# Optimization experiments

Hardware: AMD Instinct MI355X
Metric: run time of the kernel (lower is better)

The kernel has to match this reference:

```python
import jax, jax.numpy as jnp
import numpy as np

DEPTH, DIM, DIN, DM, NST, RNK, CSTEM, NCLS = 4, 64, 128, 256, 16, 8, 32, 16
EPS = 1e-5


def silu(x):
    return x * jax.nn.sigmoid(x)


def layernorm(x, g, b):
    m = x.mean(-1, keepdims=True)
    v = x.var(-1, keepdims=True)
    return (x - m) / jnp.sqrt(v + EPS) * g + b


def bn3d(x, g, b, m, v):  # eval-mode BatchNorm3d, x [B,C,T,H,W]
    s = g / jnp.sqrt(v + EPS)
    return x * s[None, :, None, None, None] + (b - m * s)[None, :, None, None, None]


def dwconv3d_same(x, w, b):  # x [B,C,T,H,W], w [C,1,3,3,3]
    y = jax.lax.conv_general_dilated(x, w, (1, 1, 1), 'SAME',
                                     feature_group_count=x.shape[1],
                                     dimension_numbers=('NCDHW', 'OIDHW', 'NCDHW'))
    return y + b[None, :, None, None, None]


def mamba(u, in_w, conv_w, conv_b, xproj_w, dtproj_w, dtproj_b, Alog, Dp, out_w):
    # u: [b, L, DIN]; mamba_ssm Mamba(d_model=DIN, d_state=16, expand=2, d_conv=4)
    b, L, _ = u.shape
    xz = u @ in_w.T                                  # [b,L,2*DM]
    x, z = jnp.split(xz, 2, axis=-1)                 # [b,L,DM] each
    # causal depthwise conv1d, kernel 4, left-pad 3
    xc = jnp.moveaxis(x, 1, 2)                       # [b,DM,L]
    xc = jnp.pad(xc, ((0, 0), (0, 0), (3, 0)))
    xc = jax.lax.conv_general_dilated(xc, conv_w, (1,), 'VALID',
                                      feature_group_count=conv_w.shape[0],
                                      dimension_numbers=('NCH', 'OIH', 'NCH'))
    xc = xc + conv_b[None, :, None]
    x = silu(jnp.moveaxis(xc, 2, 1))                 # [b,L,DM]
    dbc = x @ xproj_w.T                              # [b,L,RNK+2*NST]
    dt, Bc, Cc = jnp.split(dbc, [RNK, RNK + NST], axis=-1)
    dt = jax.nn.softplus(dt @ dtproj_w.T + dtproj_b)  # [b,L,DM]
    A = -jnp.exp(Alog)                               # [DM,NST]

    def step(h, inp):
        dt_l, u_l, B_l, C_l = inp                    # [b,DM],[b,DM],[b,NST],[b,NST]
        dA = jnp.exp(dt_l[..., None] * A)            # [b,DM,NST]
        h = dA * h + (dt_l * u_l)[..., None] * B_l[:, None, :]
        y = jnp.einsum('bdn,bn->bd', h, C_l)
        return h, y

    xs = (jnp.moveaxis(dt, 1, 0), jnp.moveaxis(x, 1, 0),
          jnp.moveaxis(Bc, 1, 0), jnp.moveaxis(Cc, 1, 0))
    h0 = jnp.zeros((b, DM, NST), x.dtype)
    _, ys = jax.lax.scan(step, h0, xs)               # ys [L,b,DM]
    y = jnp.moveaxis(ys, 0, 1) + x * Dp              # D skip
    y = y * silu(z)
    return y @ out_w.T                               # [b,L,DIN]


def setup_inputs() -> dict:
    key = jax.random.key(0)
    ks = iter(jax.random.split(key, 64))

    def rn(shape, s=0.02):
        return jax.random.normal(next(ks), shape, jnp.float32) * s

    D = DEPTH
    inp = {
        'x': jax.random.normal(next(ks), (32, 1, 32, 13, 13), jnp.float32),
        # R(2+1)D stem
        'sconv_w': rn((CSTEM, 1, 1, 3, 3), 0.1),
        'bn1_g': jnp.ones((CSTEM,)), 'bn1_b': jnp.zeros((CSTEM,)),
        'bn1_m': rn((CSTEM,), 0.1),
        'bn1_v': jax.random.uniform(next(ks), (CSTEM,), jnp.float32, 0.5, 1.5),
        'tconv_w': rn((CSTEM, 1, 3, 1, 1), 0.2),
        'bn2_g': jnp.ones((CSTEM,)), 'bn2_b': jnp.zeros((CSTEM,)),
        'bn2_m': rn((CSTEM,), 0.1),
        'bn2_v': jax.random.uniform(next(ks), (CSTEM,), jnp.float32, 0.5, 1.5),
        'last_w': rn((2 * CSTEM, CSTEM, 1, 1, 1), 0.1),
        # per-block params, stacked over depth
        'ln1_g': jnp.ones((D, DIM)), 'ln1_b': jnp.zeros((D, DIM)),
        'in_proj_w': rn((D, 2 * DIN, DIM)),
        'conv3d_w': rn((D, DIN, 1, 3, 3, 3), 0.1), 'conv3d_b': rn((D, DIN), 0.1),
        'm_in_w': rn((D, 2 * DM, DIN)),
        'm_conv_w': rn((D, DM, 1, 4), 0.2), 'm_conv_b': rn((D, DM), 0.1),
        'm_xproj_w': rn((D, RNK + 2 * NST, DM)),
        'm_dtproj_w': rn((D, DM, RNK), 0.1), 'm_dtproj_b': rn((D, DM), 0.1),
        'm_Alog': jnp.log(jax.random.uniform(next(ks), (D, DM, NST), jnp.float32, 1.0, 16.0)),
        'm_D': jnp.ones((D, DM)),
        'm_out_w': rn((D, DIN, DM)),
        'out_proj_w': rn((D, DIM, DIN)),
        'ln2_g': jnp.ones((D, DIM)), 'ln2_b': jnp.zeros((D, DIM)),
        'fc1_w': rn((D, 4 * DIM, DIM)), 'fc1_b': rn((D, 4 * DIM), 0.1),
        'fc2_w': rn((D, DIM, 4 * DIM)), 'fc2_b': rn((D, DIM), 0.1),
        'head_w': rn((NCLS, DIM)), 'head_b': jnp.zeros((NCLS,)),
    }
    return inp


def reference(x, sconv_w, bn1_g, bn1_b, bn1_m, bn1_v, tconv_w, bn2_g, bn2_b, bn2_m,
              bn2_v, last_w, ln1_g, ln1_b, in_proj_w, conv3d_w, conv3d_b, m_in_w,
              m_conv_w, m_conv_b, m_xproj_w, m_dtproj_w, m_dtproj_b, m_Alog, m_D,
              m_out_w, out_proj_w, ln2_g, ln2_b, fc1_w, fc1_b, fc2_w, fc2_b,
              head_w, head_b):
    dn = ('NCDHW', 'OIDHW', 'NCDHW')
    # R(2+1)D stem: spatial conv -> BN -> ReLU -> temporal dwconv -> BN -> ReLU -> 1x1x1
    h = jax.lax.conv_general_dilated(x, sconv_w, (1, 1, 1), 'VALID', dimension_numbers=dn)
    h = jax.nn.relu(bn3d(h, bn1_g, bn1_b, bn1_m, bn1_v))
    h = jax.lax.conv_general_dilated(h, tconv_w, (1, 1, 1), 'VALID',
                                     feature_group_count=CSTEM, dimension_numbers=dn)
    h = jax.nn.relu(bn3d(h, bn2_g, bn2_b, bn2_m, bn2_v))
    h = jax.lax.conv_general_dilated(h, last_w, (1, 1, 1), 'VALID', dimension_numbers=dn)
    xb = jnp.transpose(h, (0, 2, 3, 4, 1))  # [B, T', H', W', DIM]

    for i in range(DEPTH):
        # --- SSM branch ---
        hx = layernorm(xb, ln1_g[i], ln1_b[i])
        xz = hx @ in_proj_w[i].T                       # [B,T,H,W,2*DIN]
        xs_, z = jnp.split(xz, 2, axis=-1)
        z = silu(z)
        xc = jnp.moveaxis(xs_, 4, 1)                   # [B,DIN,T,H,W]
        xc = silu(dwconv3d_same(xc, conv3d_w[i], conv3d_b[i]))
        b, c, t, hh, ww = xc.shape
        seq = jnp.moveaxis(xc.reshape(b, c, t * hh * ww), 1, 2)  # [B,L,DIN]
        seq2 = jnp.concatenate([seq, seq[:, ::-1]], axis=0)      # [2B,L,DIN]
        y2 = mamba(seq2, m_in_w[i], m_conv_w[i], m_conv_b[i], m_xproj_w[i],
                   m_dtproj_w[i], m_dtproj_b[i], m_Alog[i], m_D[i], m_out_w[i])
        y = y2[:b] + y2[b:, ::-1]
        y = y.reshape(b, t, hh, ww, c) * z
        xb = xb + y @ out_proj_w[i].T
        # --- MLP branch ---
        h2 = layernorm(xb, ln2_g[i], ln2_b[i])
        h2 = jax.nn.gelu(h2 @ fc1_w[i].T + fc1_b[i], approximate=False)
        xb = xb + h2 @ fc2_w[i].T + fc2_b[i]

    feature = xb.mean(axis=(1, 2, 3))                  # [B, DIM]
    logits = feature @ head_w.T + head_b               # [B, NCLS]
    return (logits, feature)
```

## Files before the change

kernel.cpp:

```cpp
#include <hip/hip_runtime.h>
#include <hip/hip_bf16.h>
#include <hip/hip_fp16.h>

#define LL    3630
#define EPSV  1e-5f
#define NCH   57
#define CLEN  64

typedef short bf16x8 __attribute__((ext_vector_type(8)));
typedef float f32x4  __attribute__((ext_vector_type(4)));
typedef float f32x2  __attribute__((ext_vector_type(2)));
typedef float f32x16 __attribute__((ext_vector_type(16)));

__device__ __forceinline__ float bf2f(__hip_bfloat16 x){ return __bfloat162float(x); }
__device__ __forceinline__ __hip_bfloat16 f2bf(float x){ return __float2bfloat16(x); }
__device__ __forceinline__ float siluf(float x){ return x / (1.f + __expf(-x)); }
__device__ __forceinline__ float s2f(short s){ __hip_bfloat16 t = __builtin_bit_cast(__hip_bfloat16, s); return __bfloat162float(t); }
__device__ __forceinline__ short f2s(float x){ __hip_bfloat16 t = __float2bfloat16(x); return __builtin_bit_cast(short, t); }

__global__ __launch_bounds__(256) void convert_weights(
    const float* __restrict__ s0, const float* __restrict__ s1,
    const float* __restrict__ s2, const float* __restrict__ s3,
    const float* __restrict__ s4, const float* __restrict__ s5,
    const float* __restrict__ s6,
    __hip_bfloat16* __restrict__ dst)
{
  int gid = blockIdx.x*256 + threadIdx.x;
  float v;
  if      (gid <  65536) v = s0[gid];
  else if (gid < 327680) v = s1[gid-65536];
  else if (gid < 458752) v = s2[gid-327680];
  else if (gid < 491520) v = s3[gid-458752];
  else if (gid < 557056) v = s4[gid-491520];
  else if (gid < 622592) v = s5[gid-557056];
  else if (gid < 671744){
    int rel = gid - 622592;
    int layer = rel / 12288;
    int rr  = (rel % 12288) / 256;
    int ccol= rel & 255;
    v = (rr < 40) ? s6[layer*10240 + rr*256 + ccol] : 0.f;
  }
  else return;
  dst[gid] = f2bf(v);
}

__global__ __launch_bounds__(256) void stem1_kernel(
    const float* __restrict__ x, const float* __restrict__ w,
    const float* __restrict__ g, const float* __restrict__ bb,
    const float* __restrict__ mm, const float* __restrict__ vv,
    float* __restrict__ out, int nb, int b0)
{
  int idx = blockIdx.x*256 + threadIdx.x;
  if (idx >= nb*123904) return;
  int j = idx % 11;
  int i = (idx/11) % 11;
  int t = (idx/121) % 32;
  int c = (idx/(121*32)) % 32;
  int b = idx/(121*32*32);
  const float* xp = x + ((b0+b)*32 + t)*169;
  const float* wp = w + c*9;
  float acc = 0.f;
  #pragma unroll
  for (int di=0; di<3; ++di)
    #pragma unroll
    for (int dj=0; dj<3; ++dj)
      acc += xp[(i+di)*13 + (j+dj)] * wp[di*3+dj];
  float s = g[c]*rsqrtf(vv[c]+EPSV);
  acc = acc*s + (bb[c]-mm[c]*s);
  out[idx] = fmaxf(acc, 0.f);
}

__global__ __launch_bounds__(256) void stem2_kernel(
    const float* __restrict__ h1, const float* __restrict__ w,
    const float* __restrict__ g, const float* __restrict__ bb,
    const float* __restrict__ mm, const float* __restrict__ vv,
    float* __restrict__ out, int nb)
{
  int idx = blockIdx.x*256 + threadIdx.x;
  if (idx >= nb*116160) return;
  int ij = idx % 121;
  int t  = (idx/121) % 30;
  int c  = (idx/(121*30)) % 32;
  int b  = idx/(121*30*32);
  const float* hp = h1 + ((b*32+c)*32)*121 + ij;
  const float* wp = w + c*3;
  float acc = 0.f;
  #pragma unroll
  for (int k=0;k<3;++k) acc += hp[(t+k)*121] * wp[k];
  float s = g[c]*rsqrtf(vv[c]+EPSV);
  acc = acc*s + (bb[c]-mm[c]*s);
  out[idx] = fmaxf(acc, 0.f);
}

__global__ __launch_bounds__(256) void stem3_kernel(
    const float* __restrict__ h2, const float* __restrict__ w,
    __hip_bfloat16* __restrict__ xb, int tokens)
{
  int gid = blockIdx.x*256 + threadIdx.x;
  int cc = gid & 63;
  int tok = gid >> 6;
  if (tok >= tokens) return;
  int ij = tok % 121;
  int t  = (tok/121) % 30;
  int b  = tok/LL;
  const float* hp = h2 + ((long)b*32)*30*121 + t*121 + ij;
  const float* wp = w + cc*32;
  float acc = 0.f;
  #pragma unroll
  for (int ci=0; ci<32; ++ci) acc += hp[ci*3630] * wp[ci];
  xb[(long)tok*64+cc] = f2bf(acc);
}

__global__ __launch_bounds__(256) void ln_kernel(
    const __hip_bfloat16* __restrict__ xb, const float* __restrict__ g,
    const float* __restrict__ b2, __hip_bfloat16* __restrict__ out, int tokens)
{
  int wid = threadIdx.x >> 6, lane = threadIdx.x & 63;
  long tok = (long)blockIdx.x*4 + wid;
  if (tok >= tokens) return;
  float v = bf2f(xb[tok*64 + lane]);
  float s = v, q = v*v;
  #pragma unroll
  for (int m=1; m<64; m<<=1){ s += __shfl_xor(s,m); q += __shfl_xor(q,m); }
  float mean = s*(1.f/64.f);
  float var  = q*(1.f/64.f) - mean*mean;
  float o = (v-mean)*rsqrtf(var+EPSV)*g[lane] + b2[lane];
  out[tok*64+lane] = f2bf(o);
}

template<int EPI>
__global__ __launch_bounds__(256) void gemm_bf16(
    const __hip_bfloat16* __restrict__ A, const __hip_bfloat16* __restrict__ W,
    int K, int N, int NH, int ny, int tokens,
    __hip_bfloat16* __restrict__ out1, __hip_bfloat16* __restrict__ out2,
    const float* __restrict__ bias, const __hip_bfloat16* __restrict__ gate,
    __hip_bfloat16* __restrict__ resid,
    const float* __restrict__ lng, const float* __restrict__ lnb)
{
  int w   = threadIdx.x >> 6;
  int lane= threadIdx.x & 63;
  int r16 = lane & 15;
  int kg  = lane >> 4;
  int nwg = gridDim.x;
  int orig = blockIdx.x;
  int q = nwg >> 3, r8 = nwg & 7;
  int xcd = orig & 7, off = orig >> 3;
  int wg = (xcd < r8 ? xcd*(q+1) : r8*(q+1) + (xcd-r8)*q) + off;
  int by = wg % ny;
  long bx = wg / ny;
  long m0 = bx*128 + w*32;
  int  n0 = by*64;
  long ra0 = m0 + r16;      if (ra0 > tokens-1) ra0 = tokens-1;
  long ra1 = m0 + 16 + r16; if (ra1 > tokens-1) ra1 = tokens-1;
  f32x4 acc[2][4] = { { {0,0,0,0},{0,0,0,0},{0,0,0,0},{0,0,0,0} },
                      { {0,0,0,0},{0,0,0,0},{0,0,0,0},{0,0,0,0} } };
  for (int k0 = 0; k0 < K; k0 += 32){
    bf16x8 a0 = *reinterpret_cast<const bf16x8*>(A + ra0*K + k0 + kg*8);
    bf16x8 a1 = *reinterpret_cast<const bf16x8*>(A + ra1*K + k0 + kg*8);
    #pragma unroll
    for (int f=0; f<4; ++f){
      bf16x8 b = *reinterpret_cast<const bf16x8*>(W + (long)(n0 + f*16 + r16)*K + k0 + kg*8);
      acc[0][f] = __builtin_amdgcn_mfma_f32_16x16x32_bf16(a0, b, acc[0][f], 0, 0, 0);
      acc[1][f] = __builtin_amdgcn_mfma_f32_16x16x32_bf16(a1, b, acc[1][f], 0, 0, 0);
    }
  }
  if (EPI == 5){
    float gv[4], bv[4], biasv[4];
    #pragma unroll
    for (int f=0; f<4; ++f){
      gv[f] = lng[f*16+r16]; bv[f] = lnb[f*16+r16];
      biasv[f] = bias ? bias[f*16+r16] : 0.f;
    }
    #pragma unroll
    for (int g2=0; g2<2; ++g2){
      #pragma unroll
      for (int r=0; r<4; ++r){
        long row = m0 + g2*16 + kg*4 + r;
        bool ok = row < tokens;
        long rowc = ok ? row : (tokens-1);
        float v[4]; float s = 0.f, qq = 0.f;
        #pragma unroll
        for (int f=0; f<4; ++f){
          float t = acc[g2][f][r] + biasv[f] + bf2f(resid[rowc*64 + f*16+r16]);
          v[f] = t; s += t; qq += t*t;
        }
        #pragma unroll
        for (int m=1; m<16; m<<=1){ s += __shfl_xor(s,m); qq += __shfl_xor(qq,m); }
        float mean = s*(1.f/64.f);
        float var  = qq*(1.f/64.f) - mean*mean;
        float rstd = rsqrtf(var+EPSV);
        if (ok){
          #pragma unroll
          for (int f=0; f<4; ++f){
            resid[row*64 + f*16+r16] = f2bf(v[f]);
            out1 [row*64 + f*16+r16] = f2bf((v[f]-mean)*rstd*gv[f] + bv[f]);
          }
        }
      }
    }
    return;
  }
  #pragma unroll
  for (int g2=0; g2<2; ++g2){
    #pragma unroll
    for (int f=0; f<4; ++f){
      int col = n0 + f*16 + r16;
      #pragma unroll
      for (int r=0; r<4; ++r){
        long row = m0 + g2*16 + kg*4 + r;
        if (row >= tokens) continue;
        float v = acc[g2][f][r];
        if (EPI == 0){
          if (col < NH) out1[row*NH + col] = f2bf(v);
          else          out2[row*NH + col - NH] = f2bf(siluf(v));
        } else if (EPI == 2){
          v += bias[col];
          v = 0.5f*v*(1.f + erff(v*0.70710678118f));
          out1[row*N + col] = f2bf(v);
        } else {
          out1[row*N + col] = f2bf(v * bf2f(gate[row*N + col]));
        }
      }
    }
  }
}

__global__ __launch_bounds__(256) void dwconv3d_kernel(
    const __hip_bfloat16* __restrict__ xs, const float* __restrict__ w,
    const float* __restrict__ bias, __hip_bfloat16* __restrict__ seq, int tokens)
{
  long gid = (long)blockIdx.x*256 + threadIdx.x;
  int c = gid & 127;
  long tok = gid >> 7;
  if (tok >= tokens) return;
  int j  = tok % 11;
  int i2 = (tok/11) % 11;
  int t  = (tok/121) % 30;
  long b = tok/LL;
  const float* wc = w + c*27;
  float acc = bias[c];
  #pragma unroll
  for (int dt=0; dt<3; ++dt){
    int tt = t+dt-1; if (tt<0 || tt>=30) continue;
    #pragma unroll
    for (int di=0; di<3; ++di){
      int ii = i2+di-1; if (ii<0 || ii>=11) continue;
      #pragma unroll
      for (int dj=0; dj<3; ++dj){
        int jj = j+dj-1; if (jj<0 || jj>=11) continue;
        long t2 = (b*30+tt)*121 + ii*11 + jj;
        acc += wc[dt*9+di*3+dj] * bf2f(xs[t2*128 + c]);
      }
    }
  }
  seq[tok*128 + c] = f2bf(siluf(acc));
}

__global__ __launch_bounds__(256) void mamba_pre_scan(
    const __hip_bfloat16* __restrict__ xm,
    const float* __restrict__ cw, const float* __restrict__ cbv,
    const __hip_bfloat16* __restrict__ xpw_bf,
    const float* __restrict__ dtw, const float* __restrict__ dtbv,
    const float* __restrict__ Alog,
    __hip_bfloat16* __restrict__ ub,
    float* __restrict__ pre,
    float* __restrict__ hfin, float* __restrict__ sdt,
    int nb)
{
  __shared__ __hip_bfloat16 xcs[64][264];
  __shared__ float pres[64][44];
  int s  = blockIdx.x / NCH;
  int ch = blockIdx.x % NCH;
  int p0 = ch*CLEN;
  int b  = s % nb;
  bool fwd = s < nb;
  int d = threadIdx.x;
  const long basex = (long)b*LL*256 + d;
  const long sLL = (long)s*LL;
  {
    float w0=cw[d*4], w1=cw[d*4+1], w2=cw[d*4+2], w3=cw[d*4+3], cb=cbv[d];
    float p1=0.f, p2=0.f, p3=0.f;
    if (p0-1 >= 0) p1 = bf2f(xm[basex + (long)(fwd ? p0-1 : LL-p0  )*256]);
    if (p0-2 >= 0) p2 = bf2f(xm[basex + (long)(fwd ? p0-2 : LL+1-p0)*256]);
    if (p0-3 >= 0) p3 = bf2f(xm[basex + (long)(fwd ? p0-3 : LL+2-p0)*256]);
    for (int t=0; t<64; ++t){
      int p = p0 + t;
      float xl = 0.f;
      if (p < LL) xl = bf2f(xm[basex + (long)(fwd ? p : LL-1-p)*256]);
      float xc = w3*xl + w2*p1 + w1*p2 + w0*p3 + cb;
      p3=p2; p2=p1; p1=xl;
      __hip_bfloat16 uv = f2bf(siluf(xc));
      xcs[t][d] = uv;
      if (p < LL) ub[(sLL + p)*256 + d] = uv;
    }
  }
  __syncthreads();
  {
    int w = threadIdx.x >> 6, lane = threadIdx.x & 63;
    int r16 = lane & 15, kg = lane >> 4;
    int t0 = w*16;
    f32x4 acc[3] = { {0,0,0,0},{0,0,0,0},{0,0,0,0} };
    for (int k0=0; k0<256; k0+=32){
      bf16x8 a = *reinterpret_cast<const bf16x8*>(&xcs[t0+r16][k0+kg*8]);
      #pragma unroll
      for (int f=0; f<3; ++f){
        bf16x8 bb = *reinterpret_cast<const bf16x8*>(xpw_bf + (f*16+r16)*256 + k0 + kg*8);
        acc[f] = __builtin_amdgcn_mfma_f32_16x16x32_bf16(a, bb, acc[f], 0, 0, 0);
      }
    }
    #pragma unroll
    for (int f=0; f<3; ++f){
      int col = f*16 + r16;
      #pragma unroll
      for (int r=0; r<4; ++r){
        int tl = t0 + kg*4 + r;
        int p = p0 + tl;
        if (col < 40){
          pres[tl][col] = acc[f][r];
          if (p < LL) pre[(sLL + p)*40 + col] = acc[f][r];
        }
      }
    }
  }
  __syncthreads();
  {
    int lim = LL - p0; if (lim > CLEN) lim = CLEN;
    f32x2 a2[8], h[8];
    #pragma unroll
    for (int k=0;k<8;++k){
      a2[k] = (f32x2){ -__expf(Alog[d*16+2*k])*1.44269504f,
                       -__expf(Alog[d*16+2*k+1])*1.44269504f };
      h[k] = (f32x2){0.f, 0.f};
    }
    float dw[8];
    #pragma unroll
    for (int r=0;r<8;++r) dw[r] = dtw[d*8+r];
    float dtb_d = dtbv[d];
    float sacc = 0.f;
    for (int t=0; t<lim; ++t){
      float u = bf2f(xcs[t][d]);
      float4 r0 = *reinterpret_cast<const float4*>(&pres[t][0]);
      float4 r1 = *reinterpret_cast<const float4*>(&pres[t][4]);
      float xacc = dtb_d;
      xacc = fmaf(r0.x,dw[0],fmaf(r0.y,dw[1],fmaf(r0.z,dw[2],fmaf(r0.w,dw[3],xacc))));
      xacc = fmaf(r1.x,dw[4],fmaf(r1.y,dw[5],fmaf(r1.z,dw[6],fmaf(r1.w,dw[7],xacc))));
      float dt = (xacc > 20.f) ? xacc : __logf(1.f + __expf(xacc));
      sacc += dt;
      float4 B0 = *reinterpret_cast<const float4*>(&pres[t][8]);
      float4 B1 = *reinterpret_cast<const float4*>(&pres[t][12]);
      float4 B2 = *reinterpret_cast<const float4*>(&pres[t][16]);
      float4 B3 = *reinterpret_cast<const float4*>(&pres[t][20]);
      float Bv[16] = {B0.x,B0.y,B0.z,B0.w,B1.x,B1.y,B1.z,B1.w,
                      B2.x,B2.y,B2.z,B2.w,B3.x,B3.y,B3.z,B3.w};
      f32x2 dt2  = (f32x2){dt, dt};
      float dtu = dt*u;
      f32x2 dtu2 = (f32x2){dtu, dtu};
      #pragma unroll
      for (int k=0;k<8;++k){
        f32x2 tt = dt2*a2[k];
        f32x2 e = (f32x2){ exp2f(tt.x), exp2f(tt.y) };
        f32x2 bk = (f32x2){ Bv[2*k], Bv[2*k+1] };
        h[k] = __builtin_elementwise_fma(e, h[k], dtu2*bk);
      }
    }
    long hbase = ((long)blockIdx.x*256 + d)*16;
    #pragma unroll
    for (int k=0;k<8;++k){ hfin[hbase+2*k] = h[k].x; hfin[hbase+2*k+1] = h[k].y; }
    sdt[(long)blockIdx.x*256 + d] = sacc;
  }
}

__global__ __launch_bounds__(256) void scan_comb(
    const float* __restrict__ Alog,
    float* __restrict__ hfin, const float* __restrict__ sdt)
{
  int s = blockIdx.x >> 4, dg = blockIdx.x & 15;
  int d = dg*16 + (threadIdx.x >> 4), n = threadIdx.x & 15;
  float a2 = -__expf(Alog[d*16+n]) * 1.44269504f;
  float h = 0.f;
  for (int ch=0; ch<NCH; ++ch){
    long sc = (long)s*NCH + ch;
    long idx = (sc*256 + d)*16 + n;
    float hf = hfin[idx];
    float sd = sdt[sc*256 + d];
    hfin[idx] = h;
    h = exp2f(a2*sd)*h + hf;
  }
}

__global__ __launch_bounds__(256) void scan_p2(
    __hip_bfloat16* __restrict__ ub,
    const float* __restrict__ pre,
    const float* __restrict__ dtw, const float* __restrict__ dtbv,
    const float* __restrict__ Alog, const float* __restrict__ Dv,
    const float* __restrict__ hinit)
{
  int d = threadIdx.x;
  int sc = blockIdx.x;
  int ch = sc % NCH, s = sc / NCH;
  int l0 = ch*CLEN;
  int lim = LL - l0; if (lim > CLEN) lim = CLEN;
  f32x2 a2[8], h[8];
  long hbase = ((long)sc*256 + d)*16;
  #pragma unroll
  for (int k=0;k<8;++k){
    a2[k] = (f32x2){ -__expf(Alog[d*16+2*k])*1.44269504f,
                     -__expf(Alog[d*16+2*k+1])*1.44269504f };
    h[k] = (f32x2){ hinit[hbase+2*k], hinit[hbase+2*k+1] };
  }
  float dw[8];
  #pragma unroll
  for (int r=0;r<8;++r) dw[r] = dtw[d*8+r];
  float dtb_d = dtbv[d];
  float dpv = Dv[d];
  long tok0 = (long)s*LL + l0;
  long ui = tok0*256 + d;
  long pi = tok0*40;
  for (int l=0; l<lim; ++l){
    float u = bf2f(ub[ui]);
    float4 r0 = *reinterpret_cast<const float4*>(pre+pi);
    float4 r1 = *reinterpret_cast<const float4*>(pre+pi+4);
    float xacc = dtb_d;
    xacc = fmaf(r0.x,dw[0],fmaf(r0.y,dw[1],fmaf(r0.z,dw[2],fmaf(r0.w,dw[3],xacc))));
    xacc = fmaf(r1.x,dw[4],fmaf(r1.y,dw[5],fmaf(r1.z,dw[6],fmaf(r1.w,dw[7],xacc))));
    float dt = (xacc > 20.f) ? xacc : __logf(1.f + __expf(xacc));
    f32x16 B = *reinterpret_cast<const f32x16*>(pre+pi+8);
    f32x16 C = *reinterpret_cast<const f32x16*>(pre+pi+24);
    f32x2 dt2  = (f32x2){dt, dt};
    float dtu = dt*u;
    f32x2 dtu2 = (f32x2){dtu, dtu};
    f32x2 y2 = (f32x2){0.f, 0.f};
    #pragma unroll
    for (int k=0;k<8;++k){
      f32x2 t = dt2*a2[k];
      f32x2 e = (f32x2){ exp2f(t.x), exp2f(t.y) };
      f32x2 bk = (f32x2){ B[2*k], B[2*k+1] };
      f32x2 ck = (f32x2){ C[2*k], C[2*k+1] };
      h[k] = __builtin_elementwise_fma(e, h[k], dtu2*bk);
      y2 = __builtin_elementwise_fma(h[k], ck, y2);
    }
    float y = y2.x + y2.y;
    ub[ui] = f2bf(y + u*dpv);
    ui += 256; pi += 40;
  }
}

__global__ __launch_bounds__(256) void combine_kernel(
    const __hip_bfloat16* __restrict__ yb, const __hip_bfloat16* __restrict__ zm,
    __hip_bfloat16* __restrict__ ycomb, int tokens, int nb)
{
  long gid = (long)blockIdx.x*256 + threadIdx.x;
  long tok = gid >> 5;
  if (tok >= tokens) return;
  int c8 = (gid & 31) * 8;
  long l = tok % LL, b = tok / LL;
  bf16x8 vf = *reinterpret_cast<const bf16x8*>(yb + ( b*LL + l)*256 + c8);
  bf16x8 vb = *reinterpret_cast<const bf16x8*>(yb + ((nb+b)*LL + (LL-1-l))*256 + c8);
  bf16x8 zz = *reinterpret_cast<const bf16x8*>(zm + tok*256 + c8);
  bf16x8 out;
  #pragma unroll
  for (int k=0;k<8;++k){
    float r = (s2f(vf[k]) + s2f(vb[k])) * s2f(zz[k]);
    out[k] = f2s(r);
  }
  *reinterpret_cast<bf16x8*>(ycomb + tok*256 + c8) = out;
}

__global__ __launch_bounds__(256) void head1_kernel(
    const __hip_bfloat16* __restrict__ xb, float* __restrict__ hp)
{
  __shared__ float partial[4][64];
  int b = blockIdx.x / 30, ch = blockIdx.x % 30;
  int d = threadIdx.x & 63, part = threadIdx.x >> 6;
  float acc = 0.f;
  int lend = (ch+1)*121;
  for (int l = ch*121 + part; l < lend; l += 4)
    acc += bf2f(xb[((long)b*LL + l)*64 + d]);
  partial[part][d] = acc;
  __syncthreads();
  if (part == 0)
    hp[(b*30 + ch)*64 + d] = partial[0][d]+partial[1][d]+partial[2][d]+partial[3][d];
}

__global__ __launch_bounds__(64) void head2_kernel(
    const float* __restrict__ hp, const float* __restrict__ hw,
    const float* __restrict__ hb, float* __restrict__ out, int b0)
{
  __shared__ float feat[64];
  int b = blockIdx.x;
  int d = threadIdx.x;
  float acc = 0.f;
  #pragma unroll
  for (int ch=0; ch<30; ++ch) acc += hp[(b*30+ch)*64 + d];
  float f = acc * (1.f/3630.f);
  feat[d] = f;
  out[512 + (b0+b)*64 + d] = f;
  __syncthreads();
  if (d < 16){
    float a2 = hb[d];
    #pragma unroll
    for (int k=0; k<64; ++k) a2 += feat[k]*hw[d*64+k];
    out[(b0+b)*16 + d] = a2;
  }
}

extern "C" void kernel_launch(void* const* d_in, const int* in_sizes, int n_in,
                              void* d_out, int out_size, void* d_ws, size_t ws_size,
                              hipStream_t stream)
{
  const float* x        = (const float*)d_in[0];
  const float* sconv_w  = (const float*)d_in[1];
  const float* bn1_g    = (const float*)d_in[2];
  const float* bn1_b    = (const float*)d_in[3];
  const float* bn1_m    = (const float*)d_in[4];
  const float* bn1_v    = (const float*)d_in[5];
  const float* tconv_w  = (const float*)d_in[6];
  const float* bn2_g    = (const float*)d_in[7];
  const float* bn2_b    = (const float*)d_in[8];
  const float* bn2_m    = (const float*)d_in[9];
  const float* bn2_v    = (const float*)d_in[10];
  const float* last_w   = (const float*)d_in[11];
  const float* ln1_g    = (const float*)d_in[12];
  const float* ln1_b    = (const float*)d_in[13];
  const float* in_proj_w= (const float*)d_in[14];
  const float* conv3d_w = (const float*)d_in[15];
  const float* conv3d_b = (const float*)d_in[16];
  const float* m_in_w   = (const float*)d_in[17];
  const float* m_conv_w = (const float*)d_in[18];
  const float* m_conv_b = (const float*)d_in[19];
  const float* m_xproj_w= (const float*)d_in[20];
  const float* m_dtproj_w=(const float*)d_in[21];
  const float* m_dtproj_b=(const float*)d_in[22];
  const float* m_Alog   = (const float*)d_in[23];
  const float* m_D      = (const float*)d_in[24];
  const float* m_out_w  = (const float*)d_in[25];
  const float* out_proj_w=(const float*)d_in[26];
  const float* ln2_g    = (const float*)d_in[27];
  const float* ln2_b    = (const float*)d_in[28];
  const float* fc1_w    = (const float*)d_in[29];
  const float* fc1_b    = (const float*)d_in[30];
  const float* fc2_w    = (const float*)d_in[31];
  const float* fc2_b    = (const float*)d_in[32];
  const float* head_w   = (const float*)d_in[33];
  const float* head_b   = (const float*)d_in[34];

  const size_t WB = 1345536;
  int nb = 1;
  for (int cand = 32; cand >= 1; cand >>= 1){
    size_t TPc = (((size_t)cand*LL + 63)/64)*64;
    size_t S2c = (size_t)2*cand*LL;
    size_t need = WB + TPc*2048 + S2c*672;
    if (need <= ws_size){ nb = cand; break; }
  }
  const size_t TP  = (((size_t)nb*LL + 63)/64)*64;
  const int S2  = 2*nb;
  const size_t S2T = (size_t)S2*LL;
  const int tokens = nb*LL;

  char* ws = (char*)d_ws;
  __hip_bfloat16* wbf   = (__hip_bfloat16*)(ws);
  size_t o = WB;
  __hip_bfloat16* xb    = (__hip_bfloat16*)(ws + o); o += TP*128;
  __hip_bfloat16* hx    = (__hip_bfloat16*)(ws + o); o += TP*128;
  float*          hp    = (float*)hx;
  float*          hfin  = (float*)hx;
  __hip_bfloat16* xs    = (__hip_bfloat16*)(ws + o); o += TP*256;
  __hip_bfloat16* seq   = (__hip_bfloat16*)(ws + o); o += TP*256;
  __hip_bfloat16* ycomb = xs;
  __hip_bfloat16* zblk  = (__hip_bfloat16*)(ws + o); o += TP*256;
  __hip_bfloat16* xm    = (__hip_bfloat16*)(ws + o);
  __hip_bfloat16* yo    = xm;                        o += TP*512;
  __hip_bfloat16* zm    = (__hip_bfloat16*)(ws + o);
  __hip_bfloat16* h2m   = zm;                        o += TP*512;
  float*          pre   = (float*)(ws + o);          o += S2T*160;
  __hip_bfloat16* ybuf  = (__hip_bfloat16*)(ws + o);
  float*          h1s   = (float*)(ws + o);
  float*          h2s   = (float*)(ws + o + (size_t)nb*495616);
  float*          sdtb  = hfin + (size_t)S2*NCH*4096;

  convert_weights<<<2624, 256, 0, stream>>>(in_proj_w, m_in_w, m_out_w, out_proj_w,
                                            fc1_w, fc2_w, m_xproj_w, wbf);

  const int gM2 = (int)((TP + 127)/128);

  for (int b0 = 0; b0 < 32; b0 += nb){
    stem1_kernel<<<nb*484, 256, 0, stream>>>(x, sconv_w, bn1_g, bn1_b, bn1_m, bn1_v, h1s, nb, b0);
    stem2_kernel<<<(nb*116160+255)/256, 256, 0, stream>>>(h1s, tconv_w, bn2_g, bn2_b, bn2_m, bn2_v, h2s, nb);
    stem3_kernel<<<(tokens*64+255)/256, 256, 0, stream>>>(h2s, last_w, xb, tokens);
    ln_kernel<<<(tokens+3)/4, 256, 0, stream>>>(xb, ln1_g, ln1_b, hx, tokens);

    for (int i = 0; i < 4; ++i){
      gemm_bf16<0><<<gM2*4, 256, 0, stream>>>(hx, wbf + i*16384, 64, 256, 128, 4, tokens,
                                              xs, zblk, nullptr, nullptr, nullptr, nullptr, nullptr);
      dwconv3d_kernel<<<(tokens*128+255)/256, 256, 0, stream>>>(xs, conv3d_w + i*3456, conv3d_b + i*128, seq, tokens);
      gemm_bf16<0><<<gM2*8, 256, 0, stream>>>(seq, wbf + 65536 + i*65536, 128, 512, 256, 8, tokens,
                                              xm, zm, nullptr, nullptr, nullptr, nullptr, nullptr);
      mamba_pre_scan<<<S2*NCH, 256, 0, stream>>>(xm, m_conv_w + i*1024, m_conv_b + i*256,
                                                 wbf + 622592 + i*12288,
                                                 m_dtproj_w + i*2048, m_dtproj_b + i*256,
                                                 m_Alog + i*4096,
                                                 ybuf, pre, hfin, sdtb, nb);
      scan_comb<<<S2*16, 256, 0, stream>>>(m_Alog + i*4096, hfin, sdtb);
      scan_p2<<<S2*NCH, 256, 0, stream>>>(ybuf, pre, m_dtproj_w + i*2048, m_dtproj_b + i*256,
                                          m_Alog + i*4096, m_D + i*256, hfin);
      combine_kernel<<<(tokens*32+255)/256, 256, 0, stream>>>(ybuf, zm, ycomb, tokens, nb);
      gemm_bf16<4><<<gM2*2, 256, 0, stream>>>(ycomb, wbf + 327680 + i*32768, 256, 128, 0, 2, tokens,
                                              yo, nullptr, nullptr, zblk, nullptr, nullptr, nullptr);
      gemm_bf16<5><<<gM2, 256, 0, stream>>>(yo, wbf + 458752 + i*8192, 128, 64, 0, 1, tokens,
                                            hx, nullptr, nullptr, nullptr, xb,
                                            ln2_g + i*64, ln2_b + i*64);
      gemm_bf16<2><<<gM2*4, 256, 0, stream>>>(hx, wbf + 491520 + i*16384, 64, 256, 0, 4, tokens,
                                              h2m, nullptr, fc1_b + i*256, nullptr, nullptr, nullptr, nullptr);
      int inext = (i < 3) ? i+1 : 3;
      gemm_bf16<5><<<gM2, 256, 0, stream>>>(h2m, wbf + 557056 + i*16384, 256, 64, 0, 1, tokens,
                                            hx, nullptr, fc2_b + i*64, nullptr, xb,
                                            ln1_g + inext*64, ln1_b + inext*64);
    }
    head1_kernel<<<nb*30, 256, 0, stream>>>(xb, hp);
    head2_kernel<<<nb, 64, 0, stream>>>(hp, head_w, head_b, (float*)d_out, b0);
  }
}
```

Baseline: 6.205 ms.

## Recompute conv and x_proj in second scan pass instead of storing intermediates

The chunked selective scan now runs a single templated kernel twice. The second pass recomputes the causal conv1d, SiLU and x_proj MFMA per chunk from the in_proj output, so the fp32 dt/B/C buffer and the bf16 u buffer are no longer written to and re-read from global memory. This trades global memory traffic for repeated conv and MFMA work. The smaller workspace requirement may also allow a larger batch per iteration.

```diff
diff --git a/kernel.cpp b/kernel.cpp
--- a/kernel.cpp
+++ b/kernel.cpp
@@ -10,7 +10,6 @@
 typedef short bf16x8 __attribute__((ext_vector_type(8)));
 typedef float f32x4  __attribute__((ext_vector_type(4)));
 typedef float f32x2  __attribute__((ext_vector_type(2)));
-typedef float f32x16 __attribute__((ext_vector_type(16)));
 
 __device__ __forceinline__ float bf2f(__hip_bfloat16 x){ return __bfloat162float(x); }
 __device__ __forceinline__ __hip_bfloat16 f2bf(float x){ return __float2bfloat16(x); }
@@ -256,15 +255,15 @@
   seq[tok*128 + c] = f2bf(siluf(acc));
 }
 
-__global__ __launch_bounds__(256) void mamba_pre_scan(
+template<int PASS>
+__global__ __launch_bounds__(256) void mamba_scan(
     const __hip_bfloat16* __restrict__ xm,
     const float* __restrict__ cw, const float* __restrict__ cbv,
     const __hip_bfloat16* __restrict__ xpw_bf,
     const float* __restrict__ dtw, const float* __restrict__ dtbv,
-    const float* __restrict__ Alog,
-    __hip_bfloat16* __restrict__ ub,
-    float* __restrict__ pre,
-    float* __restrict__ hfin, float* __restrict__ sdt,
+    const float* __restrict__ Alog, const float* __restrict__ Dv,
+    float* __restrict__ hbuf, float* __restrict__ sdt,
+    __hip_bfloat16* __restrict__ yb,
     int nb)
 {
   __shared__ __hip_bfloat16 xcs[64][264];
@@ -289,9 +288,7 @@
       if (p < LL) xl = bf2f(xm[basex + (long)(fwd ? p : LL-1-p)*256]);
       float xc = w3*xl + w2*p1 + w1*p2 + w0*p3 + cb;
       p3=p2; p2=p1; p1=xl;
-      __hip_bfloat16 uv = f2bf(siluf(xc));
-      xcs[t][d] = uv;
-      if (p < LL) ub[(sLL + p)*256 + d] = uv;
+      xcs[t][d] = f2bf(siluf(xc));
     }
   }
   __syncthreads();
@@ -314,11 +311,7 @@
       #pragma unroll
       for (int r=0; r<4; ++r){
         int tl = t0 + kg*4 + r;
-        int p = p0 + tl;
-        if (col < 40){
-          pres[tl][col] = acc[f][r];
-          if (p < LL) pre[(sLL + p)*40 + col] = acc[f][r];
-        }
+        if (col < 40) pres[tl][col] = acc[f][r];
       }
     }
   }
@@ -326,16 +319,19 @@
   {
     int lim = LL - p0; if (lim > CLEN) lim = CLEN;
     f32x2 a2[8], h[8];
+    long hbase = ((long)blockIdx.x*256 + d)*16;
     #pragma unroll
     for (int k=0;k<8;++k){
       a2[k] = (f32x2){ -__expf(Alog[d*16+2*k])*1.44269504f,
                        -__expf(Alog[d*16+2*k+1])*1.44269504f };
-      h[k] = (f32x2){0.f, 0.f};
+      if (PASS == 1) h[k] = (f32x2){0.f, 0.f};
+      else           h[k] = (f32x2){ hbuf[hbase+2*k], hbuf[hbase+2*k+1] };
     }
     float dw[8];
     #pragma unroll
     for (int r=0;r<8;++r) dw[r] = dtw[d*8+r];
     float dtb_d = dtbv[d];
+    float dpv = (PASS == 2) ? Dv[d] : 0.f;
     float sacc = 0.f;
     for (int t=0; t<lim; ++t){
       float u = bf2f(xcs[t][d]);
@@ -345,7 +341,7 @@
       xacc = fmaf(r0.x,dw[0],fmaf(r0.y,dw[1],fmaf(r0.z,dw[2],fmaf(r0.w,dw[3],xacc))));
       xacc = fmaf(r1.x,dw[4],fmaf(r1.y,dw[5],fmaf(r1.z,dw[6],fmaf(r1.w,dw[7],xacc))));
       float dt = (xacc > 20.f) ? xacc : __logf(1.f + __expf(xacc));
-      sacc += dt;
+      if (PASS == 1) sacc += dt;
       float4 B0 = *reinterpret_cast<const float4*>(&pres[t][8]);
       float4 B1 = *reinterpret_cast<const float4*>(&pres[t][12]);
       float4 B2 = *reinterpret_cast<const float4*>(&pres[t][16]);
@@ -355,18 +351,39 @@
       f32x2 dt2  = (f32x2){dt, dt};
       float dtu = dt*u;
       f32x2 dtu2 = (f32x2){dtu, dtu};
+      if (PASS == 1){
+        #pragma unroll
+        for (int k=0;k<8;++k){
+          f32x2 tt = dt2*a2[k];
+          f32x2 e = (f32x2){ exp2f(tt.x), exp2f(tt.y) };
+          f32x2 bk = (f32x2){ Bv[2*k], Bv[2*k+1] };
+          h[k] = __builtin_elementwise_fma(e, h[k], dtu2*bk);
+        }
+      } else {
+        float4 C0 = *reinterpret_cast<const float4*>(&pres[t][24]);
+        float4 C1 = *reinterpret_cast<const float4*>(&pres[t][28]);
+        float4 C2 = *reinterpret_cast<const float4*>(&pres[t][32]);
+        float4 C3 = *reinterpret_cast<const float4*>(&pres[t][36]);
+        float Cv[16] = {C0.x,C0.y,C0.z,C0.w,C1.x,C1.y,C1.z,C1.w,
+                        C2.x,C2.y,C2.z,C2.w,C3.x,C3.y,C3.z,C3.w};
+        f32x2 y2 = (f32x2){0.f, 0.f};
+        #pragma unroll
+        for (int k=0;k<8;++k){
+          f32x2 tt = dt2*a2[k];
+          f32x2 e = (f32x2){ exp2f(tt.x), exp2f(tt.y) };
+          f32x2 bk = (f32x2){ Bv[2*k], Bv[2*k+1] };
+          f32x2 ck = (f32x2){ Cv[2*k], Cv[2*k+1] };
+          h[k] = __builtin_elementwise_fma(e, h[k], dtu2*bk);
+          y2 = __builtin_elementwise_fma(h[k], ck, y2);
+        }
+        yb[(sLL + p0 + t)*256 + d] = f2bf(y2.x + y2.y + u*dpv);
+      }
+    }
+    if (PASS == 1){
       #pragma unroll
-      for (int k=0;k<8;++k){
-        f32x2 tt = dt2*a2[k];
-        f32x2 e = (f32x2){ exp2f(tt.x), exp2f(tt.y) };
-        f32x2 bk = (f32x2){ Bv[2*k], Bv[2*k+1] };
-        h[k] = __builtin_elementwise_fma(e, h[k], dtu2*bk);
-      }
-    }
-    long hbase = ((long)blockIdx.x*256 + d)*16;
-    #pragma unroll
-    for (int k=0;k<8;++k){ hfin[hbase+2*k] = h[k].x; hfin[hbase+2*k+1] = h[k].y; }
-    sdt[(long)blockIdx.x*256 + d] = sacc;
+      for (int k=0;k<8;++k){ hbuf[hbase+2*k] = h[k].x; hbuf[hbase+2*k+1] = h[k].y; }
+      sdt[(long)blockIdx.x*256 + d] = sacc;
+    }
   }
 }
 
@@ -385,63 +402,6 @@
     float sd = sdt[sc*256 + d];
     hfin[idx] = h;
     h = exp2f(a2*sd)*h + hf;
-  }
-}
-
-__global__ __launch_bounds__(256) void scan_p2(
-    __hip_bfloat16* __restrict__ ub,
-    const float* __restrict__ pre,
-    const float* __restrict__ dtw, const float* __restrict__ dtbv,
-    const float* __restrict__ Alog, const float* __restrict__ Dv,
-    const float* __restrict__ hinit)
-{
-  int d = threadIdx.x;
-  int sc = blockIdx.x;
-  int ch = sc % NCH, s = sc / NCH;
-  int l0 = ch*CLEN;
-  int lim = LL - l0; if (lim > CLEN) lim = CLEN;
-  f32x2 a2[8], h[8];
-  long hbase = ((long)sc*256 + d)*16;
-  #pragma unroll
-  for (int k=0;k<8;++k){
-    a2[k] = (f32x2){ -__expf(Alog[d*16+2*k])*1.44269504f,
-                     -__expf(Alog[d*16+2*k+1])*1.44269504f };
-    h[k] = (f32x2){ hinit[hbase+2*k], hinit[hbase+2*k+1] };
-  }
-  float dw[8];
-  #pragma unroll
-  for (int r=0;r<8;++r) dw[r] = dtw[d*8+r];
-  float dtb_d = dtbv[d];
-  float dpv = Dv[d];
-  long tok0 = (long)s*LL + l0;
-  long ui = tok0*256 + d;
-  long pi = tok0*40;
-  for (int l=0; l<lim; ++l){
-    float u = bf2f(ub[ui]);
-    float4 r0 = *reinterpret_cast<const float4*>(pre+pi);
-    float4 r1 = *reinterpret_cast<const float4*>(pre+pi+4);
-    float xacc = dtb_d;
-    xacc = fmaf(r0.x,dw[0],fmaf(r0.y,dw[1],fmaf(r0.z,dw[2],fmaf(r0.w,dw[3],xacc))));
-    xacc = fmaf(r1.x,dw[4],fmaf(r1.y,dw[5],fmaf(r1.z,dw[6],fmaf(r1.w,dw[7],xacc))));
-    float dt = (xacc > 20.f) ? xacc : __logf(1.f + __expf(xacc));
-    f32x16 B = *reinterpret_cast<const f32x16*>(pre+pi+8);
-    f32x16 C = *reinterpret_cast<const f32x16*>(pre+pi+24);
-    f32x2 dt2  = (f32x2){dt, dt};
-    float dtu = dt*u;
-    f32x2 dtu2 = (f32x2){dtu, dtu};
-    f32x2 y2 = (f32x2){0.f, 0.f};
-    #pragma unroll
-    for (int k=0;k<8;++k){
-      f32x2 t = dt2*a2[k];
-      f32x2 e = (f32x2){ exp2f(t.x), exp2f(t.y) };
-      f32x2 bk = (f32x2){ B[2*k], B[2*k+1] };
-      f32x2 ck = (f32x2){ C[2*k], C[2*k+1] };
-      h[k] = __builtin_elementwise_fma(e, h[k], dtu2*bk);
-      y2 = __builtin_elementwise_fma(h[k], ck, y2);
-    }
-    float y = y2.x + y2.y;
-    ub[ui] = f2bf(y + u*dpv);
-    ui += 256; pi += 40;
   }
 }
 
@@ -549,12 +509,11 @@
   for (int cand = 32; cand >= 1; cand >>= 1){
     size_t TPc = (((size_t)cand*LL + 63)/64)*64;
     size_t S2c = (size_t)2*cand*LL;
-    size_t need = WB + TPc*2048 + S2c*672;
+    size_t need = WB + TPc*2048 + S2c*512;
     if (need <= ws_size){ nb = cand; break; }
   }
   const size_t TP  = (((size_t)nb*LL + 63)/64)*64;
   const int S2  = 2*nb;
-  const size_t S2T = (size_t)S2*LL;
   const int tokens = nb*LL;
 
   char* ws = (char*)d_ws;
@@ -572,7 +531,6 @@
   __hip_bfloat16* yo    = xm;                        o += TP*512;
   __hip_bfloat16* zm    = (__hip_bfloat16*)(ws + o);
   __hip_bfloat16* h2m   = zm;                        o += TP*512;
-  float*          pre   = (float*)(ws + o);          o += S2T*160;
   __hip_bfloat16* ybuf  = (__hip_bfloat16*)(ws + o);
   float*          h1s   = (float*)(ws + o);
   float*          h2s   = (float*)(ws + o + (size_t)nb*495616);
@@ -595,14 +553,17 @@
       dwconv3d_kernel<<<(tokens*128+255)/256, 256, 0, stream>>>(xs, conv3d_w + i*3456, conv3d_b + i*128, seq, tokens);
       gemm_bf16<0><<<gM2*8, 256, 0, stream>>>(seq, wbf + 65536 + i*65536, 128, 512, 256, 8, tokens,
                                               xm, zm, nullptr, nullptr, nullptr, nullptr, nullptr);
-      mamba_pre_scan<<<S2*NCH, 256, 0, stream>>>(xm, m_conv_w + i*1024, m_conv_b + i*256,
-                                                 wbf + 622592 + i*12288,
-                                                 m_dtproj_w + i*2048, m_dtproj_b + i*256,
-                                                 m_Alog + i*4096,
-                                                 ybuf, pre, hfin, sdtb, nb);
+      mamba_scan<1><<<S2*NCH, 256, 0, stream>>>(xm, m_conv_w + i*1024, m_conv_b + i*256,
+                                                wbf + 622592 + i*12288,
+                                                m_dtproj_w + i*2048, m_dtproj_b + i*256,
+                                                m_Alog + i*4096, m_D + i*256,
+                                                hfin, sdtb, nullptr, nb);
       scan_comb<<<S2*16, 256, 0, stream>>>(m_Alog + i*4096, hfin, sdtb);
-      scan_p2<<<S2*NCH, 256, 0, stream>>>(ybuf, pre, m_dtproj_w + i*2048, m_dtproj_b + i*256,
-                                          m_Alog + i*4096, m_D + i*256, hfin);
+      mamba_scan<2><<<S2*NCH, 256, 0, stream>>>(xm, m_conv_w + i*1024, m_conv_b + i*256,
+                                                wbf + 622592 + i*12288,
+                                                m_dtproj_w + i*2048, m_dtproj_b + i*256,
+                                                m_Alog + i*4096, m_D + i*256,
+                                                hfin, sdtb, ybuf, nb);
       combine_kernel<<<(tokens*32+255)/256, 256, 0, stream>>>(ybuf, zm, ycomb, tokens, nb);
       gemm_bf16<4><<<gM2*2, 256, 0, stream>>>(ycomb, wbf + 327680 + i*32768, 256, 128, 0, 2, tokens,
                                               yo, nullptr, nullptr, zblk, nullptr, nullptr, nullptr);
```

Result: slower. 6.545 ms (+5.5%).

## Fuse bidirectional combine into out-projection GEMM and LayerNorm into stem3

Applied to the files above, without the earlier changes.

Removes the standalone combine kernel by computing (forward + reversed backward) * z directly while staging the A tile into LDS inside a new out-projection GEMM, avoiding a write and reread of the combined activation. Also folds the first LayerNorm into stem3 via wavefront shuffles, removing a separate LN pass over xb. The new GEMM uses one workgroup per 128 rows with all 128 output columns, which lowers the number of workgroups and reads W directly from global memory without LDS staging.

```diff
diff --git a/kernel.cpp b/kernel.cpp
--- a/kernel.cpp
+++ b/kernel.cpp
@@ -94,7 +94,8 @@
 
 __global__ __launch_bounds__(256) void stem3_kernel(
     const float* __restrict__ h2, const float* __restrict__ w,
-    __hip_bfloat16* __restrict__ xb, int tokens)
+    const float* __restrict__ lng, const float* __restrict__ lnb,
+    __hip_bfloat16* __restrict__ xb, __hip_bfloat16* __restrict__ hx, int tokens)
 {
   int gid = blockIdx.x*256 + threadIdx.x;
   int cc = gid & 63;
@@ -109,23 +110,12 @@
   #pragma unroll
   for (int ci=0; ci<32; ++ci) acc += hp[ci*3630] * wp[ci];
   xb[(long)tok*64+cc] = f2bf(acc);
-}
-
-__global__ __launch_bounds__(256) void ln_kernel(
-    const __hip_bfloat16* __restrict__ xb, const float* __restrict__ g,
-    const float* __restrict__ b2, __hip_bfloat16* __restrict__ out, int tokens)
-{
-  int wid = threadIdx.x >> 6, lane = threadIdx.x & 63;
-  long tok = (long)blockIdx.x*4 + wid;
-  if (tok >= tokens) return;
-  float v = bf2f(xb[tok*64 + lane]);
-  float s = v, q = v*v;
+  float s = acc, q = acc*acc;
   #pragma unroll
   for (int m=1; m<64; m<<=1){ s += __shfl_xor(s,m); q += __shfl_xor(q,m); }
   float mean = s*(1.f/64.f);
   float var  = q*(1.f/64.f) - mean*mean;
-  float o = (v-mean)*rsqrtf(var+EPSV)*g[lane] + b2[lane];
-  out[tok*64+lane] = f2bf(o);
+  hx[(long)tok*64+cc] = f2bf((acc-mean)*rsqrtf(var+EPSV)*lng[cc] + lnb[cc]);
 }
 
 template<int EPI>
@@ -217,9 +207,77 @@
           v += bias[col];
           v = 0.5f*v*(1.f + erff(v*0.70710678118f));
           out1[row*N + col] = f2bf(v);
-        } else {
-          out1[row*N + col] = f2bf(v * bf2f(gate[row*N + col]));
         }
+      }
+    }
+  }
+}
+
+__global__ __launch_bounds__(256) void gemm_mout_fused(
+    const __hip_bfloat16* __restrict__ yb,
+    const __hip_bfloat16* __restrict__ zm,
+    const __hip_bfloat16* __restrict__ W,
+    const __hip_bfloat16* __restrict__ gate,
+    __hip_bfloat16* __restrict__ out,
+    int tokens, int nb)
+{
+  __shared__ __hip_bfloat16 at[128][136];
+  int w = threadIdx.x >> 6, lane = threadIdx.x & 63;
+  int r16 = lane & 15, kg = lane >> 4;
+  int nwg = gridDim.x;
+  int orig = blockIdx.x;
+  int q = nwg >> 3, r8 = nwg & 7;
+  int xcd = orig & 7, off = orig >> 3;
+  int wg = (xcd < r8 ? xcd*(q+1) : r8*(q+1) + (xcd-r8)*q) + off;
+  long m0 = (long)wg*128;
+  int sr  = threadIdx.x >> 1;
+  int sc0 = (threadIdx.x & 1) * 64;
+  long srow = m0 + sr; if (srow > tokens-1) srow = tokens-1;
+  long sl = srow % LL, sb = srow / LL;
+  long mrow = ((long)nb + sb)*LL + (LL-1-sl);
+  f32x4 acc[2][8];
+  #pragma unroll
+  for (int g2=0; g2<2; ++g2)
+    #pragma unroll
+    for (int f=0; f<8; ++f) acc[g2][f] = (f32x4){0,0,0,0};
+  #pragma unroll
+  for (int kh=0; kh<2; ++kh){
+    if (kh) __syncthreads();
+    #pragma unroll
+    for (int u8=0; u8<8; ++u8){
+      int c = sc0 + u8*8;
+      int cg = kh*128 + c;
+      bf16x8 vf = *reinterpret_cast<const bf16x8*>(yb + srow*256 + cg);
+      bf16x8 vb = *reinterpret_cast<const bf16x8*>(yb + mrow*256 + cg);
+      bf16x8 zz = *reinterpret_cast<const bf16x8*>(zm + srow*256 + cg);
+      bf16x8 cmb;
+      #pragma unroll
+      for (int k=0;k<8;++k) cmb[k] = f2s((s2f(vf[k]) + s2f(vb[k])) * s2f(zz[k]));
+      *reinterpret_cast<bf16x8*>(&at[sr][c]) = cmb;
+    }
+    __syncthreads();
+    #pragma unroll
+    for (int ks=0; ks<4; ++ks){
+      bf16x8 a0 = *reinterpret_cast<const bf16x8*>(&at[w*32 + r16][ks*32 + kg*8]);
+      bf16x8 a1 = *reinterpret_cast<const bf16x8*>(&at[w*32 + 16 + r16][ks*32 + kg*8]);
+      #pragma unroll
+      for (int f=0; f<8; ++f){
+        bf16x8 b = *reinterpret_cast<const bf16x8*>(W + (long)(f*16+r16)*256 + kh*128 + ks*32 + kg*8);
+        acc[0][f] = __builtin_amdgcn_mfma_f32_16x16x32_bf16(a0, b, acc[0][f], 0, 0, 0);
+        acc[1][f] = __builtin_amdgcn_mfma_f32_16x16x32_bf16(a1, b, acc[1][f], 0, 0, 0);
+      }
+    }
+  }
+  #pragma unroll
+  for (int g2=0; g2<2; ++g2){
+    #pragma unroll
+    for (int f=0; f<8; ++f){
+      int col = f*16 + r16;
+      #pragma unroll
+      for (int r=0; r<4; ++r){
+        long row = m0 + w*32 + g2*16 + kg*4 + r;
+        if (row >= tokens) continue;
+        out[row*128 + col] = f2bf(acc[g2][f][r] * bf2f(gate[row*128 + col]));
       }
     }
   }
@@ -443,27 +501,6 @@
     ub[ui] = f2bf(y + u*dpv);
     ui += 256; pi += 40;
   }
-}
-
-__global__ __launch_bounds__(256) void combine_kernel(
-    const __hip_bfloat16* __restrict__ yb, const __hip_bfloat16* __restrict__ zm,
-    __hip_bfloat16* __restrict__ ycomb, int tokens, int nb)
-{
-  long gid = (long)blockIdx.x*256 + threadIdx.x;
-  long tok = gid >> 5;
-  if (tok >= tokens) return;
-  int c8 = (gid & 31) * 8;
-  long l = tok % LL, b = tok / LL;
-  bf16x8 vf = *reinterpret_cast<const bf16x8*>(yb + ( b*LL + l)*256 + c8);
-  bf16x8 vb = *reinterpret_cast<const bf16x8*>(yb + ((nb+b)*LL + (LL-1-l))*256 + c8);
-  bf16x8 zz = *reinterpret_cast<const bf16x8*>(zm + tok*256 + c8);
-  bf16x8 out;
-  #pragma unroll
-  for (int k=0;k<8;++k){
-    float r = (s2f(vf[k]) + s2f(vb[k])) * s2f(zz[k]);
-    out[k] = f2s(r);
-  }
-  *reinterpret_cast<bf16x8*>(ycomb + tok*256 + c8) = out;
 }
 
 __global__ __launch_bounds__(256) void head1_kernel(
@@ -566,7 +603,6 @@
   float*          hfin  = (float*)hx;
   __hip_bfloat16* xs    = (__hip_bfloat16*)(ws + o); o += TP*256;
   __hip_bfloat16* seq   = (__hip_bfloat16*)(ws + o); o += TP*256;
-  __hip_bfloat16* ycomb = xs;
   __hip_bfloat16* zblk  = (__hip_bfloat16*)(ws + o); o += TP*256;
   __hip_bfloat16* xm    = (__hip_bfloat16*)(ws + o);
   __hip_bfloat16* yo    = xm;                        o += TP*512;
@@ -586,8 +622,7 @@
   for (int b0 = 0; b0 < 32; b0 += nb){
     stem1_kernel<<<nb*484, 256, 0, stream>>>(x, sconv_w, bn1_g, bn1_b, bn1_m, bn1_v, h1s, nb, b0);
     stem2_kernel<<<(nb*116160+255)/256, 256, 0, stream>>>(h1s, tconv_w, bn2_g, bn2_b, bn2_m, bn2_v, h2s, nb);
-    stem3_kernel<<<(tokens*64+255)/256, 256, 0, stream>>>(h2s, last_w, xb, tokens);
-    ln_kernel<<<(tokens+3)/4, 256, 0, stream>>>(xb, ln1_g, ln1_b, hx, tokens);
+    stem3_kernel<<<(tokens*64+255)/256, 256, 0, stream>>>(h2s, last_w, ln1_g, ln1_b, xb, hx, tokens);
 
     for (int i = 0; i < 4; ++i){
       gemm_bf16<0><<<gM2*4, 256, 0, stream>>>(hx, wbf + i*16384, 64, 256, 128, 4, tokens,
@@ -603,9 +638,8 @@
       scan_comb<<<S2*16, 256, 0, stream>>>(m_Alog + i*4096, hfin, sdtb);
       scan_p2<<<S2*NCH, 256, 0, stream>>>(ybuf, pre, m_dtproj_w + i*2048, m_dtproj_b + i*256,
                                           m_Alog + i*4096, m_D + i*256, hfin);
-      combine_kernel<<<(tokens*32+255)/256, 256, 0, stream>>>(ybuf, zm, ycomb, tokens, nb);
-      gemm_bf16<4><<<gM2*2, 256, 0, stream>>>(ycomb, wbf + 327680 + i*32768, 256, 128, 0, 2, tokens,
-                                              yo, nullptr, nullptr, zblk, nullptr, nullptr, nullptr);
+      gemm_mout_fused<<<gM2, 256, 0, stream>>>(ybuf, zm, wbf + 327680 + i*32768, zblk, yo,
+                                               tokens, nb);
       gemm_bf16<5><<<gM2, 256, 0, stream>>>(yo, wbf + 458752 + i*8192, 128, 64, 0, 1, tokens,
                                             hx, nullptr, nullptr, nullptr, xb,
                                             ln2_g + i*64, ln2_b + i*64);
```

New measurement: 6.652 ms. +7.2%, slower.
